# Performance work log

Measured on AMD Instinct MI355X. Metric: run time of the kernel, lower is better.

## Reference

```python
import jax, jax.numpy as jnp
import numpy as np

B, C_IN, L = 8, 64, 4096
C_OUT, HEADS = 64, 3
E = 524288
T_DIM = 256
N = B * L
EPS = 1e-5
NEG_SLOPE = 0.2  # PyG GATConv default negative_slope


def setup_inputs() -> dict:
    key = jax.random.key(0)
    ks = jax.random.split(key, 12)
    x = jax.random.normal(ks[0], (B, C_IN, L), jnp.float32)
    time_emb = jax.random.normal(ks[1], (B, T_DIM), jnp.float32)
    edge_index = jax.random.randint(ks[2], (2, E), 0, N, dtype=jnp.int32)
    # GATConv params: lin maps in -> heads*out; att_src/att_dst per head
    W_lin = jax.random.normal(ks[3], (C_IN, HEADS * C_OUT), jnp.float32) / np.sqrt(C_IN)
    att_src = jax.random.normal(ks[4], (1, HEADS, C_OUT), jnp.float32) / np.sqrt(C_OUT)
    att_dst = jax.random.normal(ks[5], (1, HEADS, C_OUT), jnp.float32) / np.sqrt(C_OUT)
    bias = jnp.zeros((C_OUT,), jnp.float32)
    # time projection (computed but unused in the source forward)
    tp_W = jax.random.normal(ks[6], (T_DIM, C_OUT), jnp.float32) / np.sqrt(T_DIM)
    tp_b = jnp.zeros((C_OUT,), jnp.float32)
    # BatchNorm1d affine params (training-mode batch stats)
    gamma = jnp.ones((C_OUT,), jnp.float32)
    beta = jnp.zeros((C_OUT,), jnp.float32)
    return {"x": x, "time_emb": time_emb, "edge_index": edge_index,
            "W_lin": W_lin, "att_src": att_src, "att_dst": att_dst,
            "bias": bias, "tp_W": tp_W, "tp_b": tp_b,
            "gamma": gamma, "beta": beta}


def reference(x, time_emb, edge_index, W_lin, att_src, att_dst, bias, tp_W, tp_b, gamma, beta):
    b, c, l = x.shape
    n = b * l
    # time projection: present in source but its result is never used
    _t = (time_emb @ tp_W + tp_b)[:, :, None]  # [b, C_OUT, 1] (dead)
    h = (x.reshape(-1, c) @ W_lin).reshape(n, HEADS, C_OUT)  # [N,H,C]
    a_src = (h * att_src).sum(-1)  # [N,H]
    a_dst = (h * att_dst).sum(-1)  # [N,H]
    # add self loops (PyG default add_self_loops=True)
    loops = jnp.arange(n, dtype=edge_index.dtype)
    src = jnp.concatenate([edge_index[0], loops])
    dst = jnp.concatenate([edge_index[1], loops])
    e = a_src[src] + a_dst[dst]                        # [E+N, H]
    e = jnp.where(e > 0, e, NEG_SLOPE * e)             # LeakyReLU
    emax = jax.ops.segment_max(e, dst, num_segments=n)  # every node has a self loop
    ex = jnp.exp(e - emax[dst])
    denom = jax.ops.segment_sum(ex, dst, num_segments=n)
    alpha = ex / denom[dst]                            # segment softmax over dst
    msg = alpha[:, :, None] * h[src]                   # [E+N, H, C]
    out = jax.ops.segment_sum(msg, dst, num_segments=n)  # [N,H,C]
    out = out.mean(axis=1) + bias                      # concat=False -> head mean
    # BatchNorm1d (training mode: biased batch stats)
    mu = out.mean(axis=0)
    var = ((out - mu) ** 2).mean(axis=0)
    out = (out - mu) / jnp.sqrt(var + EPS) * gamma + beta
    out = jax.nn.relu(out)
    return out.reshape(b, -1, l)
```

## Files before the change

kernel.cpp:

```cpp
#include <hip/hip_runtime.h>
#include <hip/hip_bf16.h>

#define N_NODES 32768
#define E_EDGES 524288
#define HC 192
#define NEG_SLOPE 0.2f
#define BN_EPS 1e-5f
#define PAD 64

typedef _Float16 f16;

#define GEMM_BLOCKS 1536
#define GEMM_WAVES (GEMM_BLOCKS * 4)

__device__ __forceinline__ float lrelu(float v) { return v > 0.f ? v : NEG_SLOPE * v; }

__device__ __forceinline__ float wave_sum(float v) {
#pragma unroll
    for (int off = 32; off > 0; off >>= 1) v += __shfl_xor(v, off);
    return v;
}
__device__ __forceinline__ float rlane(float v, int l) {
    return __uint_as_float(__builtin_amdgcn_readlane(__float_as_uint(v), l));
}

__global__ void k_scatter(const int4* __restrict__ src4, const int4* __restrict__ dst4,
                          int* __restrict__ cnt, unsigned short* __restrict__ csr_pad) {
    int i = blockIdx.x * blockDim.x + threadIdx.x;
    int4 s = src4[i];
    int4 d = dst4[i];
    int p0 = atomicAdd(&cnt[d.x], 1);
    int p1 = atomicAdd(&cnt[d.y], 1);
    int p2 = atomicAdd(&cnt[d.z], 1);
    int p3 = atomicAdd(&cnt[d.w], 1);
    if (p0 < PAD) csr_pad[d.x * PAD + p0] = (unsigned short)s.x;
    if (p1 < PAD) csr_pad[d.y * PAD + p1] = (unsigned short)s.y;
    if (p2 < PAD) csr_pad[d.z * PAD + p2] = (unsigned short)s.z;
    if (p3 < PAD) csr_pad[d.w * PAD + p3] = (unsigned short)s.w;
}

__global__ __launch_bounds__(256, 2) void k_gemm(
        const float* __restrict__ x, const float* __restrict__ W,
        const float* __restrict__ att_s, const float* __restrict__ att_d,
        f16* __restrict__ hh, float* __restrict__ a_src, float* __restrict__ a_dst,
        float* __restrict__ gp1, float* __restrict__ gp2) {
    if (blockIdx.x == 0) {
        float4 z = make_float4(0.f, 0.f, 0.f, 0.f);
#pragma unroll
        for (int i = 0; i < 4; i++) {
            ((float4*)gp1)[threadIdx.x * 4 + i] = z;
            ((float4*)gp2)[threadIdx.x * 4 + i] = z;
        }
    }
    const int lane  = threadIdx.x & 63;
    const int wid   = (blockIdx.x * 256 + threadIdx.x) >> 6;
    const int head  = wid / (GEMM_WAVES / 3);
    const int wslot = wid % (GEMM_WAVES / 3);
    const int c     = head * 64 + lane;

    float wcol[64];
#pragma unroll
    for (int k = 0; k < 64; k++) wcol[k] = W[k * HC + c];
    const float As = att_s[c];
    const float Ad = att_d[c];

#pragma unroll 1
    for (int n = wslot; n < N_NODES; n += (GEMM_WAVES / 3)) {
        float xv = x[(size_t)n * 64 + lane];
        float acc = 0.f;
#pragma unroll
        for (int k = 0; k < 64; k++) {
            float xk = rlane(xv, k);
            acc = fmaf(xk, wcol[k], acc);
        }
        hh[(size_t)n * HC + c] = (f16)acc;
        float s = wave_sum(acc * As);
        float d = wave_sum(acc * Ad);
        if (lane == 0) {
            a_src[n * 4 + head] = s;
            a_dst[n * 4 + head] = d;
        }
    }
}

__global__ __launch_bounds__(256) void k_node(const f16* __restrict__ hh,
                                              const float* __restrict__ a_src,
                                              const float* __restrict__ a_dst,
                                              const int* __restrict__ cnt,
                                              const unsigned short* __restrict__ csr_pad,
                                              const float* __restrict__ bias,
                                              float* __restrict__ out_pre,
                                              float* __restrict__ gp1,
                                              float* __restrict__ gp2) {
    const int lane = threadIdx.x & 63;
    const int wv = threadIdx.x >> 6;
    const int n = blockIdx.x * 4 + wv;

    int deg = cnt[n]; if (deg > PAD) deg = PAD;
    const unsigned short* __restrict__ row = csr_pad + n * PAD;

    const float ad0 = a_dst[n * 4 + 0], ad1 = a_dst[n * 4 + 1], ad2 = a_dst[n * 4 + 2];

    float ws0 = __expf(lrelu(a_src[n * 4 + 0] + ad0));
    float ws1 = __expf(lrelu(a_src[n * 4 + 1] + ad1));
    float ws2 = __expf(lrelu(a_src[n * 4 + 2] + ad2));
    float den0 = ws0, den1 = ws1, den2 = ws2;
    const f16* hn = hh + (size_t)n * HC;
    float acc0 = ws0 * (float)hn[lane];
    float acc1 = ws1 * (float)hn[64 + lane];
    float acc2 = ws2 * (float)hn[128 + lane];

    int s = 0;
    float w0 = 0.f, w1 = 0.f, w2 = 0.f;
    if (lane < deg) {
        s = (int)row[lane];
        float4 as = ((const float4*)a_src)[s];
        w0 = __expf(lrelu(as.x + ad0));
        w1 = __expf(lrelu(as.y + ad1));
        w2 = __expf(lrelu(as.z + ad2));
    }
    den0 += wave_sum(w0);
    den1 += wave_sum(w1);
    den2 += wave_sum(w2);

    int j = 0;
    for (; j + 8 <= deg; j += 8) {
#pragma unroll
        for (int u = 0; u < 8; u += 4) {
            int s0 = __builtin_amdgcn_readlane(s, j + u);
            int s1 = __builtin_amdgcn_readlane(s, j + u + 1);
            int s2 = __builtin_amdgcn_readlane(s, j + u + 2);
            int s3 = __builtin_amdgcn_readlane(s, j + u + 3);
            const f16* __restrict__ h0 = hh + (size_t)s0 * HC;
            const f16* __restrict__ h1 = hh + (size_t)s1 * HC;
            const f16* __restrict__ h2 = hh + (size_t)s2 * HC;
            const f16* __restrict__ h3 = hh + (size_t)s3 * HC;
            float v00 = (float)h0[lane], v01 = (float)h0[64 + lane], v02 = (float)h0[128 + lane];
            float v10 = (float)h1[lane], v11 = (float)h1[64 + lane], v12 = (float)h1[128 + lane];
            float v20 = (float)h2[lane], v21 = (float)h2[64 + lane], v22 = (float)h2[128 + lane];
            float v30 = (float)h3[lane], v31 = (float)h3[64 + lane], v32 = (float)h3[128 + lane];
            float w00 = rlane(w0, j + u),     w01 = rlane(w1, j + u),     w02 = rlane(w2, j + u);
            float w10 = rlane(w0, j + u + 1), w11 = rlane(w1, j + u + 1), w12 = rlane(w2, j + u + 1);
            float w20 = rlane(w0, j + u + 2), w21 = rlane(w1, j + u + 2), w22 = rlane(w2, j + u + 2);
            float w30 = rlane(w0, j + u + 3), w31 = rlane(w1, j + u + 3), w32 = rlane(w2, j + u + 3);
            acc0 = fmaf(w00, v00, acc0); acc0 = fmaf(w10, v10, acc0);
            acc0 = fmaf(w20, v20, acc0); acc0 = fmaf(w30, v30, acc0);
            acc1 = fmaf(w01, v01, acc1); acc1 = fmaf(w11, v11, acc1);
            acc1 = fmaf(w21, v21, acc1); acc1 = fmaf(w31, v31, acc1);
            acc2 = fmaf(w02, v02, acc2); acc2 = fmaf(w12, v12, acc2);
            acc2 = fmaf(w22, v22, acc2); acc2 = fmaf(w32, v32, acc2);
        }
    }
    for (; j < deg; j++) {
        int sa = __builtin_amdgcn_readlane(s, j);
        const f16* __restrict__ ha = hh + (size_t)sa * HC;
        float wa0 = rlane(w0, j), wa1 = rlane(w1, j), wa2 = rlane(w2, j);
        acc0 = fmaf(wa0, (float)ha[lane], acc0);
        acc1 = fmaf(wa1, (float)ha[64 + lane], acc1);
        acc2 = fmaf(wa2, (float)ha[128 + lane], acc2);
    }

    float outv = (acc0 / den0 + acc1 / den1 + acc2 / den2) * (1.0f / 3.0f) + bias[lane];
    out_pre[n * 64 + lane] = outv;

    __shared__ float ls[4][64], lq[4][64];
    ls[wv][lane] = outv;
    lq[wv][lane] = outv * outv;
    __syncthreads();
    if (threadIdx.x < 64) {
        int t = threadIdx.x;
        float s_ = ls[0][t] + ls[1][t] + ls[2][t] + ls[3][t];
        float q_ = lq[0][t] + lq[1][t] + lq[2][t] + lq[3][t];
        int slice = blockIdx.x & 63;
        atomicAdd(&gp1[slice * 64 + t], s_);
        atomicAdd(&gp2[slice * 64 + t], q_);
    }
}

#define APPLY_BLOCKS 512
__global__ __launch_bounds__(256) void k_apply(const float4* __restrict__ out_pre4,
                                               const float* __restrict__ gp1,
                                               const float* __restrict__ gp2,
                                               const float* __restrict__ gamma,
                                               const float* __restrict__ beta,
                                               float4* __restrict__ out4) {
    __shared__ float sc[64], sh[64];
    if (threadIdx.x < 64) {
        int t = threadIdx.x;
        float s = 0.f, q = 0.f;
        for (int i = 0; i < 64; i++) { s += gp1[i * 64 + t]; q += gp2[i * 64 + t]; }
        const float inv_n = 1.0f / (float)N_NODES;
        float mu = s * inv_n;
        float var = q * inv_n - mu * mu;
        float invstd = 1.0f / sqrtf(var + BN_EPS);
        float scale = invstd * gamma[t];
        sc[t] = scale;
        sh[t] = beta[t] - mu * scale;
    }
    __syncthreads();
    const int total = N_NODES * 64 / 4;
    for (int idx = blockIdx.x * 256 + threadIdx.x; idx < total; idx += APPLY_BLOCKS * 256) {
        int c0 = (idx * 4) & 63;
        float4 v = out_pre4[idx];
        float4 r;
        r.x = fmaxf(v.x * sc[c0 + 0] + sh[c0 + 0], 0.f);
        r.y = fmaxf(v.y * sc[c0 + 1] + sh[c0 + 1], 0.f);
        r.z = fmaxf(v.z * sc[c0 + 2] + sh[c0 + 2], 0.f);
        r.w = fmaxf(v.w * sc[c0 + 3] + sh[c0 + 3], 0.f);
        out4[idx] = r;
    }
}

extern "C" void kernel_launch(void* const* d_in, const int* in_sizes, int n_in,
                              void* d_out, int out_size, void* d_ws, size_t ws_size,
                              hipStream_t stream) {
    const float* x     = (const float*)d_in[0];
    const int*   ei    = (const int*)d_in[2];
    const float* W     = (const float*)d_in[3];
    const float* att_s = (const float*)d_in[4];
    const float* att_d = (const float*)d_in[5];
    const float* bias  = (const float*)d_in[6];
    const float* gamma = (const float*)d_in[9];
    const float* beta  = (const float*)d_in[10];
    float* out = (float*)d_out;

    char* ws = (char*)d_ws;
    size_t off = 0;
    auto alloc = [&](size_t bytes) -> void* {
        void* p = ws + off;
        off += (bytes + 255) & ~(size_t)255;
        return p;
    };
    f16*            hh      = (f16*)alloc((size_t)N_NODES * HC * 2);
    float*          a_src   = (float*)alloc((size_t)N_NODES * 4 * 4);
    float*          a_dst   = (float*)alloc((size_t)N_NODES * 4 * 4);
    int*            cnt     = (int*)alloc((size_t)N_NODES * 4);
    unsigned short* csr_pad = (unsigned short*)alloc((size_t)N_NODES * PAD * 2);
    float*          out_pre = (float*)alloc((size_t)N_NODES * 64 * 4);
    float*          gp1     = (float*)alloc(64 * 64 * 4);
    float*          gp2     = (float*)alloc(64 * 64 * 4);

    hipMemsetAsync(cnt, 0, (size_t)N_NODES * 4, stream);

    k_scatter<<<E_EDGES / 4 / 256, 256, 0, stream>>>((const int4*)ei,
                                                     (const int4*)(ei + E_EDGES),
                                                     cnt, csr_pad);
    k_gemm<<<GEMM_BLOCKS, 256, 0, stream>>>(x, W, att_s, att_d, hh, a_src, a_dst,
                                            gp1, gp2);
    k_node<<<N_NODES / 4, 256, 0, stream>>>(hh, a_src, a_dst, cnt, csr_pad, bias,
                                            out_pre, gp1, gp2);
    k_apply<<<APPLY_BLOCKS, 256, 0, stream>>>((const float4*)out_pre, gp1, gp2,
                                              gamma, beta, (float4*)out);
}
```

Measured before the change: 175.6 us.

## Fuse all stages into one cooperative persistent kernel with grid syncs

Replaces the memset plus four separate launches (scatter, GEMM, node aggregation, BN apply) with a single cooperative kernel of 255 blocks that uses grid.sync between phases. Each wave accumulates BN partial sums in registers across the nodes it handles and issues one atomic at the end, instead of per-block shared-memory reductions. This removes launch gaps and kernel boundaries. In exchange the grid is limited to 255 blocks, which lowers occupancy for the latency-bound gather and GEMM phases, and it adds the cost of three grid-wide barriers.

Result: slower. 394.2 us (+124.5%).

```diff
diff --git a/kernel.cpp b/kernel.cpp
--- a/kernel.cpp
+++ b/kernel.cpp
@@ -1,5 +1,8 @@
 #include <hip/hip_runtime.h>
 #include <hip/hip_bf16.h>
+#include <hip/hip_cooperative_groups.h>
+
+namespace cg = cooperative_groups;
 
 #define N_NODES 32768
 #define E_EDGES 524288
@@ -8,10 +11,12 @@
 #define BN_EPS 1e-5f
 #define PAD 64
 
+#define NB 255
+#define NT 256
+#define NWAVES (NB * 4)
+#define WPH (NWAVES / 3)
+
 typedef _Float16 f16;
-
-#define GEMM_BLOCKS 1536
-#define GEMM_WAVES (GEMM_BLOCKS * 4)
 
 __device__ __forceinline__ float lrelu(float v) { return v > 0.f ? v : NEG_SLOPE * v; }
 
@@ -24,113 +29,104 @@
     return __uint_as_float(__builtin_amdgcn_readlane(__float_as_uint(v), l));
 }
 
-__global__ void k_scatter(const int4* __restrict__ src4, const int4* __restrict__ dst4,
-                          int* __restrict__ cnt, unsigned short* __restrict__ csr_pad) {
-    int i = blockIdx.x * blockDim.x + threadIdx.x;
-    int4 s = src4[i];
-    int4 d = dst4[i];
-    int p0 = atomicAdd(&cnt[d.x], 1);
-    int p1 = atomicAdd(&cnt[d.y], 1);
-    int p2 = atomicAdd(&cnt[d.z], 1);
-    int p3 = atomicAdd(&cnt[d.w], 1);
-    if (p0 < PAD) csr_pad[d.x * PAD + p0] = (unsigned short)s.x;
-    if (p1 < PAD) csr_pad[d.y * PAD + p1] = (unsigned short)s.y;
-    if (p2 < PAD) csr_pad[d.z * PAD + p2] = (unsigned short)s.z;
-    if (p3 < PAD) csr_pad[d.w * PAD + p3] = (unsigned short)s.w;
-}
-
-__global__ __launch_bounds__(256, 2) void k_gemm(
+__global__ __launch_bounds__(256) void k_all(
         const float* __restrict__ x, const float* __restrict__ W,
         const float* __restrict__ att_s, const float* __restrict__ att_d,
+        const float* __restrict__ bias, const float* __restrict__ gamma,
+        const float* __restrict__ beta,
+        const int4* __restrict__ src4, const int4* __restrict__ dst4,
+        int* __restrict__ cnt, unsigned short* __restrict__ csr_pad,
         f16* __restrict__ hh, float* __restrict__ a_src, float* __restrict__ a_dst,
-        float* __restrict__ gp1, float* __restrict__ gp2) {
-    if (blockIdx.x == 0) {
-        float4 z = make_float4(0.f, 0.f, 0.f, 0.f);
+        float* __restrict__ out_pre, float* __restrict__ gp1, float* __restrict__ gp2,
+        float* __restrict__ out) {
+    cg::grid_group grid = cg::this_grid();
+    const int tid  = blockIdx.x * NT + threadIdx.x;
+    const int lane = threadIdx.x & 63;
+    const int wid  = tid >> 6;
+
+    for (int i = tid; i < N_NODES; i += NB * NT) cnt[i] = 0;
+    if (tid < 4096) { gp1[tid] = 0.f; gp2[tid] = 0.f; }
+    grid.sync();
+
+    {
+        const int head  = wid / WPH;
+        const int wslot = wid % WPH;
+        const int c     = head * 64 + lane;
+
+        float wcol[64];
 #pragma unroll
-        for (int i = 0; i < 4; i++) {
-            ((float4*)gp1)[threadIdx.x * 4 + i] = z;
-            ((float4*)gp2)[threadIdx.x * 4 + i] = z;
-        }
-    }
-    const int lane  = threadIdx.x & 63;
-    const int wid   = (blockIdx.x * 256 + threadIdx.x) >> 6;
-    const int head  = wid / (GEMM_WAVES / 3);
-    const int wslot = wid % (GEMM_WAVES / 3);
-    const int c     = head * 64 + lane;
-
-    float wcol[64];
+        for (int k = 0; k < 64; k++) wcol[k] = W[k * HC + c];
+        const float As = att_s[c];
+        const float Ad = att_d[c];
+
+#pragma unroll 1
+        for (int n = wslot; n < N_NODES; n += WPH) {
+            float xv = x[(size_t)n * 64 + lane];
+            float acc = 0.f;
 #pragma unroll
-    for (int k = 0; k < 64; k++) wcol[k] = W[k * HC + c];
-    const float As = att_s[c];
-    const float Ad = att_d[c];
-
-#pragma unroll 1
-    for (int n = wslot; n < N_NODES; n += (GEMM_WAVES / 3)) {
-        float xv = x[(size_t)n * 64 + lane];
-        float acc = 0.f;
-#pragma unroll
-        for (int k = 0; k < 64; k++) {
-            float xk = rlane(xv, k);
-            acc = fmaf(xk, wcol[k], acc);
-        }
-        hh[(size_t)n * HC + c] = (f16)acc;
-        float s = wave_sum(acc * As);
-        float d = wave_sum(acc * Ad);
-        if (lane == 0) {
-            a_src[n * 4 + head] = s;
-            a_dst[n * 4 + head] = d;
-        }
-    }
-}
-
-__global__ __launch_bounds__(256) void k_node(const f16* __restrict__ hh,
-                                              const float* __restrict__ a_src,
-                                              const float* __restrict__ a_dst,
-                                              const int* __restrict__ cnt,
-                                              const unsigned short* __restrict__ csr_pad,
-                                              const float* __restrict__ bias,
-                                              float* __restrict__ out_pre,
-                                              float* __restrict__ gp1,
-                                              float* __restrict__ gp2) {
-    const int lane = threadIdx.x & 63;
-    const int wv = threadIdx.x >> 6;
-    const int n = blockIdx.x * 4 + wv;
-
-    int deg = cnt[n]; if (deg > PAD) deg = PAD;
-    const unsigned short* __restrict__ row = csr_pad + n * PAD;
-
-    const float ad0 = a_dst[n * 4 + 0], ad1 = a_dst[n * 4 + 1], ad2 = a_dst[n * 4 + 2];
-
-    float ws0 = __expf(lrelu(a_src[n * 4 + 0] + ad0));
-    float ws1 = __expf(lrelu(a_src[n * 4 + 1] + ad1));
-    float ws2 = __expf(lrelu(a_src[n * 4 + 2] + ad2));
-    float den0 = ws0, den1 = ws1, den2 = ws2;
-    const f16* hn = hh + (size_t)n * HC;
-    float acc0 = ws0 * (float)hn[lane];
-    float acc1 = ws1 * (float)hn[64 + lane];
-    float acc2 = ws2 * (float)hn[128 + lane];
-
-    int s = 0;
-    float w0 = 0.f, w1 = 0.f, w2 = 0.f;
-    if (lane < deg) {
-        s = (int)row[lane];
-        float4 as = ((const float4*)a_src)[s];
-        w0 = __expf(lrelu(as.x + ad0));
-        w1 = __expf(lrelu(as.y + ad1));
-        w2 = __expf(lrelu(as.z + ad2));
-    }
-    den0 += wave_sum(w0);
-    den1 += wave_sum(w1);
-    den2 += wave_sum(w2);
-
-    int j = 0;
-    for (; j + 8 <= deg; j += 8) {
-#pragma unroll
-        for (int u = 0; u < 8; u += 4) {
-            int s0 = __builtin_amdgcn_readlane(s, j + u);
-            int s1 = __builtin_amdgcn_readlane(s, j + u + 1);
-            int s2 = __builtin_amdgcn_readlane(s, j + u + 2);
-            int s3 = __builtin_amdgcn_readlane(s, j + u + 3);
+            for (int k = 0; k < 64; k++) {
+                float xk = rlane(xv, k);
+                acc = fmaf(xk, wcol[k], acc);
+            }
+            hh[(size_t)n * HC + c] = (f16)acc;
+            float s = wave_sum(acc * As);
+            float d = wave_sum(acc * Ad);
+            if (lane == 0) {
+                a_src[n * 4 + head] = s;
+                a_dst[n * 4 + head] = d;
+            }
+        }
+    }
+
+    for (int i = tid; i < E_EDGES / 4; i += NB * NT) {
+        int4 s = src4[i];
+        int4 d = dst4[i];
+        int p0 = atomicAdd(&cnt[d.x], 1);
+        int p1 = atomicAdd(&cnt[d.y], 1);
+        int p2 = atomicAdd(&cnt[d.z], 1);
+        int p3 = atomicAdd(&cnt[d.w], 1);
+        if (p0 < PAD) csr_pad[d.x * PAD + p0] = (unsigned short)s.x;
+        if (p1 < PAD) csr_pad[d.y * PAD + p1] = (unsigned short)s.y;
+        if (p2 < PAD) csr_pad[d.z * PAD + p2] = (unsigned short)s.z;
+        if (p3 < PAD) csr_pad[d.w * PAD + p3] = (unsigned short)s.w;
+    }
+    grid.sync();
+
+    float bnS = 0.f, bnQ = 0.f;
+    const float bi = bias[lane];
+    for (int n = wid; n < N_NODES; n += NWAVES) {
+        int deg = cnt[n]; if (deg > PAD) deg = PAD;
+        const unsigned short* __restrict__ row = csr_pad + n * PAD;
+
+        const float ad0 = a_dst[n * 4 + 0], ad1 = a_dst[n * 4 + 1], ad2 = a_dst[n * 4 + 2];
+        float ws0 = __expf(lrelu(a_src[n * 4 + 0] + ad0));
+        float ws1 = __expf(lrelu(a_src[n * 4 + 1] + ad1));
+        float ws2 = __expf(lrelu(a_src[n * 4 + 2] + ad2));
+        float den0 = ws0, den1 = ws1, den2 = ws2;
+        const f16* hn = hh + (size_t)n * HC;
+        float acc0 = ws0 * (float)hn[lane];
+        float acc1 = ws1 * (float)hn[64 + lane];
+        float acc2 = ws2 * (float)hn[128 + lane];
+
+        int s = 0;
+        float w0 = 0.f, w1 = 0.f, w2 = 0.f;
+        if (lane < deg) {
+            s = (int)row[lane];
+            float4 as = ((const float4*)a_src)[s];
+            w0 = __expf(lrelu(as.x + ad0));
+            w1 = __expf(lrelu(as.y + ad1));
+            w2 = __expf(lrelu(as.z + ad2));
+        }
+        den0 += wave_sum(w0);
+        den1 += wave_sum(w1);
+        den2 += wave_sum(w2);
+
+        int j = 0;
+        for (; j + 4 <= deg; j += 4) {
+            int s0 = __builtin_amdgcn_readlane(s, j);
+            int s1 = __builtin_amdgcn_readlane(s, j + 1);
+            int s2 = __builtin_amdgcn_readlane(s, j + 2);
+            int s3 = __builtin_amdgcn_readlane(s, j + 3);
             const f16* __restrict__ h0 = hh + (size_t)s0 * HC;
             const f16* __restrict__ h1 = hh + (size_t)s1 * HC;
             const f16* __restrict__ h2 = hh + (size_t)s2 * HC;
@@ -139,10 +135,10 @@
             float v10 = (float)h1[lane], v11 = (float)h1[64 + lane], v12 = (float)h1[128 + lane];
             float v20 = (float)h2[lane], v21 = (float)h2[64 + lane], v22 = (float)h2[128 + lane];
             float v30 = (float)h3[lane], v31 = (float)h3[64 + lane], v32 = (float)h3[128 + lane];
-            float w00 = rlane(w0, j + u),     w01 = rlane(w1, j + u),     w02 = rlane(w2, j + u);
-            float w10 = rlane(w0, j + u + 1), w11 = rlane(w1, j + u + 1), w12 = rlane(w2, j + u + 1);
-            float w20 = rlane(w0, j + u + 2), w21 = rlane(w1, j + u + 2), w22 = rlane(w2, j + u + 2);
-            float w30 = rlane(w0, j + u + 3), w31 = rlane(w1, j + u + 3), w32 = rlane(w2, j + u + 3);
+            float w00 = rlane(w0, j),     w01 = rlane(w1, j),     w02 = rlane(w2, j);
+            float w10 = rlane(w0, j + 1), w11 = rlane(w1, j + 1), w12 = rlane(w2, j + 1);
+            float w20 = rlane(w0, j + 2), w21 = rlane(w1, j + 2), w22 = rlane(w2, j + 2);
+            float w30 = rlane(w0, j + 3), w31 = rlane(w1, j + 3), w32 = rlane(w2, j + 3);
             acc0 = fmaf(w00, v00, acc0); acc0 = fmaf(w10, v10, acc0);
             acc0 = fmaf(w20, v20, acc0); acc0 = fmaf(w30, v30, acc0);
             acc1 = fmaf(w01, v01, acc1); acc1 = fmaf(w11, v11, acc1);
@@ -150,40 +146,24 @@
             acc2 = fmaf(w02, v02, acc2); acc2 = fmaf(w12, v12, acc2);
             acc2 = fmaf(w22, v22, acc2); acc2 = fmaf(w32, v32, acc2);
         }
-    }
-    for (; j < deg; j++) {
-        int sa = __builtin_amdgcn_readlane(s, j);
-        const f16* __restrict__ ha = hh + (size_t)sa * HC;
-        float wa0 = rlane(w0, j), wa1 = rlane(w1, j), wa2 = rlane(w2, j);
-        acc0 = fmaf(wa0, (float)ha[lane], acc0);
-        acc1 = fmaf(wa1, (float)ha[64 + lane], acc1);
-        acc2 = fmaf(wa2, (float)ha[128 + lane], acc2);
-    }
-
-    float outv = (acc0 / den0 + acc1 / den1 + acc2 / den2) * (1.0f / 3.0f) + bias[lane];
-    out_pre[n * 64 + lane] = outv;
-
-    __shared__ float ls[4][64], lq[4][64];
-    ls[wv][lane] = outv;
-    lq[wv][lane] = outv * outv;
-    __syncthreads();
-    if (threadIdx.x < 64) {
-        int t = threadIdx.x;
-        float s_ = ls[0][t] + ls[1][t] + ls[2][t] + ls[3][t];
-        float q_ = lq[0][t] + lq[1][t] + lq[2][t] + lq[3][t];
-        int slice = blockIdx.x & 63;
-        atomicAdd(&gp1[slice * 64 + t], s_);
-        atomicAdd(&gp2[slice * 64 + t], q_);
-    }
-}
-
-#define APPLY_BLOCKS 512
-__global__ __launch_bounds__(256) void k_apply(const float4* __restrict__ out_pre4,
-                                               const float* __restrict__ gp1,
-                                               const float* __restrict__ gp2,
-                                               const float* __restrict__ gamma,
-                                               const float* __restrict__ beta,
-                                               float4* __restrict__ out4) {
+        for (; j < deg; j++) {
+            int sa = __builtin_amdgcn_readlane(s, j);
+            const f16* __restrict__ ha = hh + (size_t)sa * HC;
+            float wa0 = rlane(w0, j), wa1 = rlane(w1, j), wa2 = rlane(w2, j);
+            acc0 = fmaf(wa0, (float)ha[lane], acc0);
+            acc1 = fmaf(wa1, (float)ha[64 + lane], acc1);
+            acc2 = fmaf(wa2, (float)ha[128 + lane], acc2);
+        }
+
+        float outv = (acc0 / den0 + acc1 / den1 + acc2 / den2) * (1.0f / 3.0f) + bi;
+        out_pre[n * 64 + lane] = outv;
+        bnS += outv;
+        bnQ += outv * outv;
+    }
+    atomicAdd(&gp1[(wid & 63) * 64 + lane], bnS);
+    atomicAdd(&gp2[(wid & 63) * 64 + lane], bnQ);
+    grid.sync();
+
     __shared__ float sc[64], sh[64];
     if (threadIdx.x < 64) {
         int t = threadIdx.x;
@@ -198,10 +178,12 @@
         sh[t] = beta[t] - mu * scale;
     }
     __syncthreads();
+    const float4* __restrict__ pre4 = (const float4*)out_pre;
+    float4* __restrict__ out4 = (float4*)out;
     const int total = N_NODES * 64 / 4;
-    for (int idx = blockIdx.x * 256 + threadIdx.x; idx < total; idx += APPLY_BLOCKS * 256) {
+    for (int idx = tid; idx < total; idx += NB * NT) {
         int c0 = (idx * 4) & 63;
-        float4 v = out_pre4[idx];
+        float4 v = pre4[idx];
         float4 r;
         r.x = fmaxf(v.x * sc[c0 + 0] + sh[c0 + 0], 0.f);
         r.y = fmaxf(v.y * sc[c0 + 1] + sh[c0 + 1], 0.f);
@@ -240,15 +222,18 @@
     float*          gp1     = (float*)alloc(64 * 64 * 4);
     float*          gp2     = (float*)alloc(64 * 64 * 4);
 
-    hipMemsetAsync(cnt, 0, (size_t)N_NODES * 4, stream);
-
-    k_scatter<<<E_EDGES / 4 / 256, 256, 0, stream>>>((const int4*)ei,
-                                                     (const int4*)(ei + E_EDGES),
-                                                     cnt, csr_pad);
-    k_gemm<<<GEMM_BLOCKS, 256, 0, stream>>>(x, W, att_s, att_d, hh, a_src, a_dst,
-                                            gp1, gp2);
-    k_node<<<N_NODES / 4, 256, 0, stream>>>(hh, a_src, a_dst, cnt, csr_pad, bias,
-                                            out_pre, gp1, gp2);
-    k_apply<<<APPLY_BLOCKS, 256, 0, stream>>>((const float4*)out_pre, gp1, gp2,
-                                              gamma, beta, (float4*)out);
-}
+    const int4* src4 = (const int4*)ei;
+    const int4* dst4 = (const int4*)(ei + E_EDGES);
+
+    void* args[] = {
+        (void*)&x, (void*)&W, (void*)&att_s, (void*)&att_d,
+        (void*)&bias, (void*)&gamma, (void*)&beta,
+        (void*)&src4, (void*)&dst4,
+        (void*)&cnt, (void*)&csr_pad,
+        (void*)&hh, (void*)&a_src, (void*)&a_dst,
+        (void*)&out_pre, (void*)&gp1, (void*)&gp2,
+        (void*)&out
+    };
+    hipLaunchCooperativeKernel(reinterpret_cast<void*>(k_all),
+                               dim3(NB), dim3(NT), args, 0, stream);
+}
```

## Fuse edge scatter into GEMM kernel via interleaved block roles

Applied to the files above, without the earlier changes.

Merges the CSR scatter kernel and the projection GEMM kernel into one launch. Every fourth block does the edge bucketing with atomics and the other blocks run the GEMM, so the two independent stages run at the same time and one launch boundary goes away. It also adds an occupancy hint of 4 to the node aggregation kernel, which may force register spilling.

After: 161.6 us. -8.0%, faster.

```diff
diff --git a/kernel.cpp b/kernel.cpp
--- a/kernel.cpp
+++ b/kernel.cpp
@@ -10,8 +10,8 @@
 
 typedef _Float16 f16;
 
-#define GEMM_BLOCKS 1536
-#define GEMM_WAVES (GEMM_BLOCKS * 4)
+#define FUSED_BLOCKS 2048
+#define GEMM_WAVES (1536 * 4)
 
 __device__ __forceinline__ float lrelu(float v) { return v > 0.f ? v : NEG_SLOPE * v; }
 
@@ -24,36 +24,38 @@
     return __uint_as_float(__builtin_amdgcn_readlane(__float_as_uint(v), l));
 }
 
-__global__ void k_scatter(const int4* __restrict__ src4, const int4* __restrict__ dst4,
-                          int* __restrict__ cnt, unsigned short* __restrict__ csr_pad) {
-    int i = blockIdx.x * blockDim.x + threadIdx.x;
-    int4 s = src4[i];
-    int4 d = dst4[i];
-    int p0 = atomicAdd(&cnt[d.x], 1);
-    int p1 = atomicAdd(&cnt[d.y], 1);
-    int p2 = atomicAdd(&cnt[d.z], 1);
-    int p3 = atomicAdd(&cnt[d.w], 1);
-    if (p0 < PAD) csr_pad[d.x * PAD + p0] = (unsigned short)s.x;
-    if (p1 < PAD) csr_pad[d.y * PAD + p1] = (unsigned short)s.y;
-    if (p2 < PAD) csr_pad[d.z * PAD + p2] = (unsigned short)s.z;
-    if (p3 < PAD) csr_pad[d.w * PAD + p3] = (unsigned short)s.w;
-}
-
-__global__ __launch_bounds__(256, 2) void k_gemm(
+__global__ __launch_bounds__(256, 2) void k_fused(
+        const int4* __restrict__ src4, const int4* __restrict__ dst4,
+        int* __restrict__ cnt, unsigned short* __restrict__ csr_pad,
         const float* __restrict__ x, const float* __restrict__ W,
         const float* __restrict__ att_s, const float* __restrict__ att_d,
         f16* __restrict__ hh, float* __restrict__ a_src, float* __restrict__ a_dst,
         float* __restrict__ gp1, float* __restrict__ gp2) {
-    if (blockIdx.x == 0) {
-        float4 z = make_float4(0.f, 0.f, 0.f, 0.f);
-#pragma unroll
-        for (int i = 0; i < 4; i++) {
-            ((float4*)gp1)[threadIdx.x * 4 + i] = z;
-            ((float4*)gp2)[threadIdx.x * 4 + i] = z;
-        }
-    }
+    if ((blockIdx.x & 3) == 0) {
+        int i = (blockIdx.x >> 2) * 256 + threadIdx.x;
+        int4 s = src4[i];
+        int4 d = dst4[i];
+        int p0 = atomicAdd(&cnt[d.x], 1);
+        int p1 = atomicAdd(&cnt[d.y], 1);
+        int p2 = atomicAdd(&cnt[d.z], 1);
+        int p3 = atomicAdd(&cnt[d.w], 1);
+        if (p0 < PAD) csr_pad[d.x * PAD + p0] = (unsigned short)s.x;
+        if (p1 < PAD) csr_pad[d.y * PAD + p1] = (unsigned short)s.y;
+        if (p2 < PAD) csr_pad[d.z * PAD + p2] = (unsigned short)s.z;
+        if (p3 < PAD) csr_pad[d.w * PAD + p3] = (unsigned short)s.w;
+        if (blockIdx.x == 0) {
+            float4 z = make_float4(0.f, 0.f, 0.f, 0.f);
+#pragma unroll
+            for (int i2 = 0; i2 < 4; i2++) {
+                ((float4*)gp1)[threadIdx.x * 4 + i2] = z;
+                ((float4*)gp2)[threadIdx.x * 4 + i2] = z;
+            }
+        }
+        return;
+    }
+    const int gbid  = blockIdx.x - (blockIdx.x >> 2) - 1;
     const int lane  = threadIdx.x & 63;
-    const int wid   = (blockIdx.x * 256 + threadIdx.x) >> 6;
+    const int wid   = (gbid * 256 + threadIdx.x) >> 6;
     const int head  = wid / (GEMM_WAVES / 3);
     const int wslot = wid % (GEMM_WAVES / 3);
     const int c     = head * 64 + lane;
@@ -83,15 +85,16 @@
     }
 }
 
-__global__ __launch_bounds__(256) void k_node(const f16* __restrict__ hh,
-                                              const float* __restrict__ a_src,
-                                              const float* __restrict__ a_dst,
-                                              const int* __restrict__ cnt,
-                                              const unsigned short* __restrict__ csr_pad,
-                                              const float* __restrict__ bias,
-                                              float* __restrict__ out_pre,
-                                              float* __restrict__ gp1,
-                                              float* __restrict__ gp2) {
+__global__ __launch_bounds__(256, 4) void k_node(
+        const f16* __restrict__ hh,
+        const float* __restrict__ a_src,
+        const float* __restrict__ a_dst,
+        const int* __restrict__ cnt,
+        const unsigned short* __restrict__ csr_pad,
+        const float* __restrict__ bias,
+        float* __restrict__ out_pre,
+        float* __restrict__ gp1,
+        float* __restrict__ gp2) {
     const int lane = threadIdx.x & 63;
     const int wv = threadIdx.x >> 6;
     const int n = blockIdx.x * 4 + wv;
@@ -242,11 +245,11 @@
 
     hipMemsetAsync(cnt, 0, (size_t)N_NODES * 4, stream);
 
-    k_scatter<<<E_EDGES / 4 / 256, 256, 0, stream>>>((const int4*)ei,
-                                                     (const int4*)(ei + E_EDGES),
-                                                     cnt, csr_pad);
-    k_gemm<<<GEMM_BLOCKS, 256, 0, stream>>>(x, W, att_s, att_d, hh, a_src, a_dst,
-                                            gp1, gp2);
+    k_fused<<<FUSED_BLOCKS, 256, 0, stream>>>((const int4*)ei,
+                                              (const int4*)(ei + E_EDGES),
+                                              cnt, csr_pad,
+                                              x, W, att_s, att_d, hh, a_src, a_dst,
+                                              gp1, gp2);
     k_node<<<N_NODES / 4, 256, 0, stream>>>(hh, a_src, a_dst, cnt, csr_pad, bias,
                                             out_pre, gp1, gp2);
     k_apply<<<APPLY_BLOCKS, 256, 0, stream>>>((const float4*)out_pre, gp1, gp2,
```
